# Optimization experiments

Measured on AMD Instinct MI355X. Metric: run time of the kernel, lower is better.

Reference implementation:

```python
import jax, jax.numpy as jnp
import numpy as np

N = 50000
E = 1600000
IN = 128
HID = 128
OUT = 64
NL = 200000
NEG_SLOPE = 0.2


def _glorot(key, shape):
    fan_in, fan_out = shape[0], shape[-1]
    s = jnp.sqrt(6.0 / (fan_in + fan_out))
    return jax.random.uniform(key, shape, jnp.float32, -s, s)


def setup_inputs() -> dict:
    key = jax.random.key(0)
    ks = jax.random.split(key, 16)
    x = jax.random.normal(ks[0], (N, IN), jnp.float32)
    edge_index = jax.random.randint(ks[1], (2, E), 0, N, dtype=jnp.int32)
    edge_label_index = jax.random.randint(ks[2], (2, NL), 0, N, dtype=jnp.int32)
    return {
        "x": x,
        "edge_index": edge_index,
        "edge_label_index": edge_label_index,
        "W1": _glorot(ks[3], (IN, HID)),  "a1s": _glorot(ks[4], (HID,)),  "a1d": _glorot(ks[5], (HID,)),  "b1": jnp.zeros((HID,), jnp.float32),
        "W2": _glorot(ks[6], (HID, HID)), "a2s": _glorot(ks[7], (HID,)),  "a2d": _glorot(ks[8], (HID,)),  "b2": jnp.zeros((HID,), jnp.float32),
        "W3": _glorot(ks[9], (HID, HID)), "a3s": _glorot(ks[10], (HID,)), "a3d": _glorot(ks[11], (HID,)), "b3": jnp.zeros((HID,), jnp.float32),
        "W4": _glorot(ks[12], (HID, OUT)), "b4": jnp.zeros((OUT,), jnp.float32),
    }


def _add_self_loops(edge_index, n):
    loop = jnp.arange(n, dtype=edge_index.dtype)
    return jnp.concatenate([edge_index, jnp.stack([loop, loop])], axis=1)


def gat_conv(x, edge_index, W, a_s, a_d, b):
    """PyG GATConv, heads=1, add_self_loops=True: gather, LeakyReLU score,
    segment softmax over destination nodes, scatter-add aggregate."""
    n = x.shape[0]
    ei = _add_self_loops(edge_index, n)
    src, dst = ei[0], ei[1]
    h = x @ W                                    # [N, H]
    e = jax.nn.leaky_relu((h @ a_s)[src] + (h @ a_d)[dst], NEG_SLOPE)  # [E']
    m = jax.ops.segment_max(e, dst, num_segments=n)
    p = jnp.exp(e - m[dst])
    s = jax.ops.segment_sum(p, dst, num_segments=n)
    alpha = p / s[dst]                           # segment softmax
    out = jax.ops.segment_sum(h[src] * alpha[:, None], dst, num_segments=n)
    return out + b


def gcn_conv(x, edge_index, W, b):
    """PyG GCNConv: self-loops + symmetric degree normalization."""
    n = x.shape[0]
    ei = _add_self_loops(edge_index, n)
    src, dst = ei[0], ei[1]
    h = x @ W
    deg = jax.ops.segment_sum(jnp.ones(src.shape, h.dtype), dst, num_segments=n)
    dinv = jax.lax.rsqrt(deg)
    norm = dinv[src] * dinv[dst]                 # [E']
    out = jax.ops.segment_sum(h[src] * norm[:, None], dst, num_segments=n)
    return out + b


def reference(x, edge_index, edge_label_index,
              W1, a1s, a1d, b1, W2, a2s, a2d, b2,
              W3, a3s, a3d, b3, W4, b4):
    h = jax.nn.relu(gat_conv(x, edge_index, W1, a1s, a1d, b1))
    h = jax.nn.relu(gat_conv(h, edge_index, W2, a2s, a2d, b2))
    h = jax.nn.relu(gat_conv(h, edge_index, W3, a3s, a3d, b3))
    z = gcn_conv(h, edge_index, W4, b4)          # [N, OUT]
    # decode: dot product of endpoint embeddings -> link logits [NL]
    return (z[edge_label_index[0]] * z[edge_label_index[1]]).sum(axis=-1)
```

## Files before the change

kernel.cpp:

```cpp
#include <hip/hip_runtime.h>
#include <hip/hip_fp16.h>
#include <math.h>

#define NN   50000
#define NE   1600000
#define DHID 128
#define DOUTC 64
#define NLBL 200000
#define CAP  80
#define NEG  0.2f
#define NBK  196
#define CAPB 8800
#define CHK  4096

typedef unsigned short u16;


__global__ __launch_bounds__(256) void k_zero(int* __restrict__ gcnt) {
    int i = threadIdx.x;
    if (i < NBK) gcnt[i] = 0;
}

__global__ __launch_bounds__(256) void k_bin(const int* __restrict__ ei,
                                             int* __restrict__ gcnt,
                                             unsigned* __restrict__ bins) {
    __shared__ int cntL[NBK];
    __shared__ int curL[NBK];
    const int tid = threadIdx.x;
    const int e0 = blockIdx.x * CHK + tid * 16;
    const bool act = (e0 + 15) < NE;

    unsigned pk[16];
    int bb[16];
    if (act) {
#pragma unroll
        for (int g = 0; g < 4; ++g) {
            int4 s4 = *(const int4*)&ei[e0 + g * 4];
            int4 d4 = *(const int4*)&ei[NE + e0 + g * 4];
            int sa[4] = {s4.x, s4.y, s4.z, s4.w};
            int da[4] = {d4.x, d4.y, d4.z, d4.w};
#pragma unroll
            for (int k = 0; k < 4; ++k) {
                int idx = g * 4 + k;
                bb[idx] = da[k] >> 8;
                pk[idx] = (unsigned)sa[k] | ((unsigned)(da[k] & 255) << 16);
            }
        }
    }
    for (int i = tid; i < NBK; i += 256) cntL[i] = 0;
    __syncthreads();
    if (act) {
#pragma unroll
        for (int k = 0; k < 16; ++k) atomicAdd(&cntL[bb[k]], 1);
    }
    __syncthreads();
    for (int i = tid; i < NBK; i += 256) curL[i] = atomicAdd(&gcnt[i], cntL[i]);
    __syncthreads();
    if (act) {
#pragma unroll
        for (int k = 0; k < 16; ++k) {
            int off = atomicAdd(&curL[bb[k]], 1);
            bins[(size_t)bb[k] * CAPB + off] = pk[k];
        }
    }
}

__global__ __launch_bounds__(256) void k_build(const unsigned* __restrict__ bins,
                                               const int* __restrict__ gcnt,
                                               int* __restrict__ cnt,
                                               u16* __restrict__ csr) {
    __shared__ u16 rows[256 * CAP];
    __shared__ int cur[256];
    const int b = blockIdx.x, tid = threadIdx.x;
    const int d0 = b << 8;
    const int nd = min(256, NN - d0);
    if (tid < nd) { cur[tid] = 1; rows[tid * CAP] = (u16)(d0 + tid); }
    __syncthreads();
    const int n = gcnt[b];
    for (int i = tid; i < n; i += 256) {
        unsigned v = bins[(size_t)b * CAPB + i];
        int s = v & 0xFFFF, dl = v >> 16;
        int pos = atomicAdd(&cur[dl], 1);
        if (pos < CAP) rows[dl * CAP + pos] = (u16)s;
    }
    __syncthreads();
    const unsigned* rw = (const unsigned*)rows;
    unsigned* cw = (unsigned*)(csr + (size_t)d0 * CAP);
    const int tot = nd * (CAP / 2);
    for (int i = tid; i < tot; i += 256) cw[i] = rw[i];
    if (tid < nd) cnt[d0 + tid] = cur[tid];
}


template <int NOUT, bool ATTN>
__global__ __launch_bounds__(256) void gemm_k(const float* __restrict__ A,
                                              const float* __restrict__ W,
                                              __half* __restrict__ C16,
                                              const float* __restrict__ a_s,
                                              const float* __restrict__ a_d,
                                              float* __restrict__ asv,
                                              float* __restrict__ adv, int M) {
    constexpr int BM = 64, BK = 32, TM = 4, TN = NOUT / 16;
    __shared__ float As[BM][36];
    __shared__ float Ws[BK][NOUT];
    const int tid = threadIdx.x;
    const int tx = tid & 15, ty = tid >> 4;
    const int row0 = blockIdx.x * BM;

    float acc[TM][TN];
#pragma unroll
    for (int i = 0; i < TM; ++i)
#pragma unroll
        for (int j = 0; j < TN; ++j) acc[i][j] = 0.f;

    for (int k0 = 0; k0 < 128; k0 += BK) {
        {
            int r = tid >> 3;
            int c = (tid & 7) * 4;
#pragma unroll
            for (int rr = 0; rr < BM; rr += 32) {
                int grow = row0 + r + rr;
                float4 v = make_float4(0.f, 0.f, 0.f, 0.f);
                if (grow < M) v = *(const float4*)&A[(size_t)grow * 128 + k0 + c];
                *(float4*)&As[r + rr][c] = v;
            }
        }
        {
            constexpr int TOT4 = BK * NOUT / 4;
#pragma unroll
            for (int i4 = tid; i4 < TOT4; i4 += 256) {
                int kk = (i4 * 4) / NOUT;
                int cc = (i4 * 4) % NOUT;
                *(float4*)&Ws[kk][cc] = *(const float4*)&W[(size_t)(k0 + kk) * NOUT + cc];
            }
        }
        __syncthreads();
#pragma unroll
        for (int k4 = 0; k4 < BK; k4 += 4) {
            float a4[TM][4];
#pragma unroll
            for (int i = 0; i < TM; ++i) {
                float4 v = *(const float4*)&As[ty * TM + i][k4];
                a4[i][0] = v.x; a4[i][1] = v.y; a4[i][2] = v.z; a4[i][3] = v.w;
            }
#pragma unroll
            for (int kk = 0; kk < 4; ++kk) {
                int k = k4 + kk;
                float rw[TN];
                if (NOUT == 128) {
                    float4 w0 = *(const float4*)&Ws[k][tx * 4];
                    float4 w1 = *(const float4*)&Ws[k][64 + tx * 4];
                    rw[0] = w0.x; rw[1] = w0.y; rw[2] = w0.z; rw[3] = w0.w;
                    rw[4] = w1.x; rw[5] = w1.y; rw[6] = w1.z; rw[7] = w1.w;
                } else {
                    float4 w0 = *(const float4*)&Ws[k][tx * 4];
                    rw[0] = w0.x; rw[1] = w0.y; rw[2] = w0.z; rw[3] = w0.w;
                }
#pragma unroll
                for (int i = 0; i < TM; ++i)
#pragma unroll
                    for (int j = 0; j < TN; ++j) acc[i][j] = fmaf(a4[i][kk], rw[j], acc[i][j]);
            }
        }
        __syncthreads();
    }
#pragma unroll
    for (int i = 0; i < TM; ++i) {
        int grow = row0 + ty * TM + i;
        if (grow < M) {
            __half2 p0 = __floats2half2_rn(acc[i][0], acc[i][1]);
            __half2 p1 = __floats2half2_rn(acc[i][2], acc[i][3]);
            __half2* cp = (__half2*)&C16[(size_t)grow * NOUT + tx * 4];
            cp[0] = p0; cp[1] = p1;
            if (NOUT == 128) {
                __half2 p2 = __floats2half2_rn(acc[i][4], acc[i][5]);
                __half2 p3 = __floats2half2_rn(acc[i][6], acc[i][7]);
                __half2* cq = (__half2*)&C16[(size_t)grow * NOUT + 64 + tx * 4];
                cq[0] = p2; cq[1] = p3;
            }
        }
    }
    if (ATTN) {
        float4 s0 = *(const float4*)&a_s[tx * 4];
        float4 s1 = *(const float4*)&a_s[64 + tx * 4];
        float4 d0 = *(const float4*)&a_d[tx * 4];
        float4 d1 = *(const float4*)&a_d[64 + tx * 4];
#pragma unroll
        for (int i = 0; i < TM; ++i) {
            float ps = acc[i][0] * s0.x + acc[i][1] * s0.y + acc[i][2] * s0.z + acc[i][3] * s0.w
                     + acc[i][4] * s1.x + acc[i][5] * s1.y + acc[i][6] * s1.z + acc[i][7] * s1.w;
            float pd = acc[i][0] * d0.x + acc[i][1] * d0.y + acc[i][2] * d0.z + acc[i][3] * d0.w
                     + acc[i][4] * d1.x + acc[i][5] * d1.y + acc[i][6] * d1.z + acc[i][7] * d1.w;
#pragma unroll
            for (int off = 1; off < 16; off <<= 1) {
                ps += __shfl_xor(ps, off);
                pd += __shfl_xor(pd, off);
            }
            int grow = row0 + ty * TM + i;
            if (tx == 0 && grow < M) { asv[grow] = ps; adv[grow] = pd; }
        }
    }
}

__device__ inline void fma_h8(uint4 u, float al, float* acc) {
    float2 f0 = __half22float2(*(__half2*)&u.x);
    float2 f1 = __half22float2(*(__half2*)&u.y);
    float2 f2 = __half22float2(*(__half2*)&u.z);
    float2 f3 = __half22float2(*(__half2*)&u.w);
    acc[0] = fmaf(al, f0.x, acc[0]);
    acc[1] = fmaf(al, f0.y, acc[1]);
    acc[2] = fmaf(al, f1.x, acc[2]);
    acc[3] = fmaf(al, f1.y, acc[3]);
    acc[4] = fmaf(al, f2.x, acc[4]);
    acc[5] = fmaf(al, f2.y, acc[5]);
    acc[6] = fmaf(al, f3.x, acc[6]);
    acc[7] = fmaf(al, f3.y, acc[7]);
}


__global__ __launch_bounds__(256) void k_gat_agg(const __half* __restrict__ h,
                                                 const int* __restrict__ cnt,
                                                 const u16* __restrict__ csr,
                                                 const float* __restrict__ asv,
                                                 const float* __restrict__ adv,
                                                 const float* __restrict__ bias,
                                                 float* __restrict__ outp) {
    int lane = threadIdx.x & 63, wv = threadIdx.x >> 6;
    int d = blockIdx.x * 4 + wv;
    if (d >= NN) return;
    int deg = cnt[d]; if (deg > CAP) deg = CAP;
    const float advd = adv[d];
    const u16* rowp = csr + (size_t)d * CAP;

    int j0 = lane, j1 = lane + 64;
    int s0 = 0, s1 = 0;
    float e0 = -INFINITY, e1 = -INFINITY;
    if (j0 < deg) {
        s0 = rowp[j0];
        float t = asv[s0] + advd;
        e0 = (t >= 0.f) ? t : NEG * t;
    }
    if (j1 < deg) {
        s1 = rowp[j1];
        float t = asv[s1] + advd;
        e1 = (t >= 0.f) ? t : NEG * t;
    }
    float m = fmaxf(e0, e1);
#pragma unroll
    for (int off = 32; off; off >>= 1) m = fmaxf(m, __shfl_xor(m, off));
    float p0 = (j0 < deg) ? __expf(e0 - m) : 0.f;
    float p1 = (j1 < deg) ? __expf(e1 - m) : 0.f;
    float s = p0 + p1;
#pragma unroll
    for (int off = 32; off; off >>= 1) s += __shfl_xor(s, off);
    float inv = 1.f / s;
    float a0 = p0 * inv, a1 = p1 * inv;

    int slot = lane >> 3, r = lane & 7;
    float acc[16];
#pragma unroll
    for (int k = 0; k < 16; ++k) acc[k] = 0.f;

    for (int base = 0; base < deg; base += 8) {
        int idx = base + slot;
        int lsrc = idx & 63;
        float alA = __shfl(a0, lsrc);
        float alB = __shfl(a1, lsrc);
        int   sjA = __shfl(s0, lsrc);
        int   sjB = __shfl(s1, lsrc);
        bool ok = idx < deg;
        float al = ok ? ((idx < 64) ? alA : alB) : 0.f;
        int   sj = ok ? ((idx < 64) ? sjA : sjB) : 0;
        const uint4* hp = (const uint4*)&h[(size_t)sj * 128 + r * 16];
        uint4 ua = hp[0];
        uint4 ub = hp[1];
        fma_h8(ua, al, acc);
        fma_h8(ub, al, acc + 8);
    }
#pragma unroll
    for (int k = 0; k < 16; ++k) {
        acc[k] += __shfl_xor(acc[k], 8);
        acc[k] += __shfl_xor(acc[k], 16);
        acc[k] += __shfl_xor(acc[k], 32);
    }
    if (slot == 0) {
        float o[16];
#pragma unroll
        for (int k = 0; k < 16; ++k) o[k] = fmaxf(acc[k] + bias[r * 16 + k], 0.f);
        float4* op = (float4*)&outp[(size_t)d * 128 + r * 16];
        op[0] = make_float4(o[0],  o[1],  o[2],  o[3]);
        op[1] = make_float4(o[4],  o[5],  o[6],  o[7]);
        op[2] = make_float4(o[8],  o[9],  o[10], o[11]);
        op[3] = make_float4(o[12], o[13], o[14], o[15]);
    }
}


__global__ __launch_bounds__(256) void k_gcn_agg(const __half* __restrict__ h,
                                                 const int* __restrict__ cnt,
                                                 const u16* __restrict__ csr,
                                                 const float* __restrict__ bias,
                                                 float* __restrict__ z) {
    int lane = threadIdx.x & 63, wv = threadIdx.x >> 6;
    int d = blockIdx.x * 4 + wv;
    if (d >= NN) return;
    int degc = cnt[d];
    int deg = degc > CAP ? CAP : degc;
    float did = rsqrtf((float)degc);
    const u16* rowp = csr + (size_t)d * CAP;

    int j0 = lane, j1 = lane + 64;
    int s0 = 0, s1 = 0;
    float n0 = 0.f, n1 = 0.f;
    if (j0 < deg) { s0 = rowp[j0]; n0 = rsqrtf((float)cnt[s0]) * did; }
    if (j1 < deg) { s1 = rowp[j1]; n1 = rsqrtf((float)cnt[s1]) * did; }

    int slot = lane >> 3, r = lane & 7;
    float acc[8];
#pragma unroll
    for (int k = 0; k < 8; ++k) acc[k] = 0.f;

    for (int base = 0; base < deg; base += 8) {
        int idx = base + slot;
        int lsrc = idx & 63;
        float nA = __shfl(n0, lsrc);
        float nB = __shfl(n1, lsrc);
        int  sjA = __shfl(s0, lsrc);
        int  sjB = __shfl(s1, lsrc);
        bool ok = idx < deg;
        float nm = ok ? ((idx < 64) ? nA : nB) : 0.f;
        int   sj = ok ? ((idx < 64) ? sjA : sjB) : 0;
        uint4 u = *(const uint4*)&h[(size_t)sj * 64 + r * 8];
        fma_h8(u, nm, acc);
    }
#pragma unroll
    for (int k = 0; k < 8; ++k) {
        acc[k] += __shfl_xor(acc[k], 8);
        acc[k] += __shfl_xor(acc[k], 16);
        acc[k] += __shfl_xor(acc[k], 32);
    }
    if (slot == 0) {
        float4 b0 = *(const float4*)&bias[r * 8];
        float4 b1 = *(const float4*)&bias[r * 8 + 4];
        float4* zp = (float4*)&z[(size_t)d * 64 + r * 8];
        zp[0] = make_float4(acc[0] + b0.x, acc[1] + b0.y, acc[2] + b0.z, acc[3] + b0.w);
        zp[1] = make_float4(acc[4] + b1.x, acc[5] + b1.y, acc[6] + b1.z, acc[7] + b1.w);
    }
}


__global__ __launch_bounds__(256) void k_decode(const float* __restrict__ z,
                                                const int* __restrict__ eli,
                                                float* __restrict__ outp) {
    int lane = threadIdx.x & 63, wv = threadIdx.x >> 6;
    int g = lane >> 4, r = lane & 15;
    int idx = (blockIdx.x * 4 + wv) * 4 + g;
    if (idx >= NLBL) return;
    int a = eli[idx], b = eli[NLBL + idx];
    float4 za = *(const float4*)&z[(size_t)a * 64 + r * 4];
    float4 zb = *(const float4*)&z[(size_t)b * 64 + r * 4];
    float v = za.x * zb.x + za.y * zb.y + za.z * zb.z + za.w * zb.w;
#pragma unroll
    for (int off = 8; off; off >>= 1) v += __shfl_xor(v, off);
    if (r == 0) outp[idx] = v;
}


extern "C" void kernel_launch(void* const* d_in, const int* in_sizes, int n_in,
                              void* d_out, int out_size, void* d_ws, size_t ws_size,
                              hipStream_t stream) {
    const float* x   = (const float*)d_in[0];
    const int*   ei  = (const int*)d_in[1];
    const int*   eli = (const int*)d_in[2];
    const float* W1 = (const float*)d_in[3];
    const float* a1s = (const float*)d_in[4];
    const float* a1d = (const float*)d_in[5];
    const float* b1 = (const float*)d_in[6];
    const float* W2 = (const float*)d_in[7];
    const float* a2s = (const float*)d_in[8];
    const float* a2d = (const float*)d_in[9];
    const float* b2 = (const float*)d_in[10];
    const float* W3 = (const float*)d_in[11];
    const float* a3s = (const float*)d_in[12];
    const float* a3d = (const float*)d_in[13];
    const float* b3 = (const float*)d_in[14];
    const float* W4 = (const float*)d_in[15];
    const float* b4 = (const float*)d_in[16];
    float* outp = (float*)d_out;

    char* p = (char*)d_ws;
    auto alloc = [&](size_t bytes) -> char* {
        char* r = p;
        p += (bytes + 255) & ~(size_t)255;
        return r;
    };
    int*   cnt  = (int*)alloc((size_t)NN * 4);
    u16*   csr  = (u16*)alloc((size_t)NN * CAP * 2);
    int*   gcnt = (int*)alloc((size_t)NBK * 4);
    float* asv  = (float*)alloc((size_t)NN * 4);
    float* advv = (float*)alloc((size_t)NN * 4);
    __half* G   = (__half*)alloc((size_t)NN * 128 * 2);
    float* Bu1  = (float*)alloc((size_t)NN * 128 * 4);
    float* Bu2  = (float*)alloc((size_t)NN * 128 * 4);
    unsigned* bins = (unsigned*)Bu2;

    const int gBin  = (NE + CHK - 1) / CHK;
    const int gGemm = (NN + 63) / 64;
    const int gNode = (NN + 3) / 4;
    const int gDec  = (NLBL + 15) / 16;

    k_zero<<<1, 256, 0, stream>>>(gcnt);
    k_bin<<<gBin, 256, 0, stream>>>(ei, gcnt, bins);
    k_build<<<NBK, 256, 0, stream>>>(bins, gcnt, cnt, csr);

    gemm_k<128, true><<<gGemm, 256, 0, stream>>>(x, W1, G, a1s, a1d, asv, advv, NN);
    k_gat_agg<<<gNode, 256, 0, stream>>>(G, cnt, csr, asv, advv, b1, Bu1);

    gemm_k<128, true><<<gGemm, 256, 0, stream>>>(Bu1, W2, G, a2s, a2d, asv, advv, NN);
    k_gat_agg<<<gNode, 256, 0, stream>>>(G, cnt, csr, asv, advv, b2, Bu2);

    gemm_k<128, true><<<gGemm, 256, 0, stream>>>(Bu2, W3, G, a3s, a3d, asv, advv, NN);
    k_gat_agg<<<gNode, 256, 0, stream>>>(G, cnt, csr, asv, advv, b3, Bu1);

    gemm_k<64, false><<<gGemm, 256, 0, stream>>>(Bu1, W4, G, nullptr, nullptr, nullptr, nullptr, NN);
    k_gcn_agg<<<gNode, 256, 0, stream>>>(G, cnt, csr, b4, Bu2);

    k_decode<<<gDec, 256, 0, stream>>>(Bu2, eli, outp);
}
```

Measured before the change: 455.6 us.

## Use fp16 MFMA for dense transforms and store layer activations in half

Replaces the scalar FP32 tiled GEMM with a kernel that puts the transposed weights in shared memory as fp16 and computes with 16x16x32 f16 MFMA instructions, keeping the fused attention-score reduction. The input features are cast to fp16 by a new kernel, and GAT aggregation outputs are written as fp16, which halves the activation traffic between layers. The aim is to remove FP32 ALU-bound GEMM time and reduce memory bandwidth. In exchange it adds a cast pass and lowers the precision of the inputs and intermediates.

New measurement: 444.1 us. 1.03x faster.

```diff
diff --git a/kernel.cpp b/kernel.cpp
--- a/kernel.cpp
+++ b/kernel.cpp
@@ -14,6 +14,8 @@
 #define CHK  4096
 
 typedef unsigned short u16;
+typedef _Float16 half8 __attribute__((ext_vector_type(8)));
+typedef float floatx4 __attribute__((ext_vector_type(4)));
 
 
 __global__ __launch_bounds__(256) void k_zero(int* __restrict__ gcnt) {
@@ -92,112 +94,104 @@
 }
 
 
+__global__ __launch_bounds__(256) void k_cast(const float* __restrict__ x,
+                                              __half* __restrict__ x16) {
+    int i = (blockIdx.x * 256 + threadIdx.x) * 4;
+    if (i < NN * 128) {
+        float4 v = *(const float4*)&x[i];
+        __half2 h0 = __floats2half2_rn(v.x, v.y);
+        __half2 h1 = __floats2half2_rn(v.z, v.w);
+        uint2 u;
+        __builtin_memcpy(&u.x, &h0, 4);
+        __builtin_memcpy(&u.y, &h1, 4);
+        *(uint2*)&x16[i] = u;
+    }
+}
+
+
 template <int NOUT, bool ATTN>
-__global__ __launch_bounds__(256) void gemm_k(const float* __restrict__ A,
-                                              const float* __restrict__ W,
-                                              __half* __restrict__ C16,
-                                              const float* __restrict__ a_s,
-                                              const float* __restrict__ a_d,
-                                              float* __restrict__ asv,
-                                              float* __restrict__ adv, int M) {
-    constexpr int BM = 64, BK = 32, TM = 4, TN = NOUT / 16;
-    __shared__ float As[BM][36];
-    __shared__ float Ws[BK][NOUT];
+__global__ __launch_bounds__(256) void gemm_mfma(const __half* __restrict__ A16,
+                                                 const float* __restrict__ W,
+                                                 __half* __restrict__ C16,
+                                                 const float* __restrict__ a_s,
+                                                 const float* __restrict__ a_d,
+                                                 float* __restrict__ asv,
+                                                 float* __restrict__ adv, int M) {
+    constexpr int CT = NOUT / 16;
+    __shared__ _Float16 Wt[NOUT][136];
     const int tid = threadIdx.x;
-    const int tx = tid & 15, ty = tid >> 4;
-    const int row0 = blockIdx.x * BM;
-
-    float acc[TM][TN];
-#pragma unroll
-    for (int i = 0; i < TM; ++i)
-#pragma unroll
-        for (int j = 0; j < TN; ++j) acc[i][j] = 0.f;
-
-    for (int k0 = 0; k0 < 128; k0 += BK) {
-        {
-            int r = tid >> 3;
-            int c = (tid & 7) * 4;
-#pragma unroll
-            for (int rr = 0; rr < BM; rr += 32) {
-                int grow = row0 + r + rr;
-                float4 v = make_float4(0.f, 0.f, 0.f, 0.f);
-                if (grow < M) v = *(const float4*)&A[(size_t)grow * 128 + k0 + c];
-                *(float4*)&As[r + rr][c] = v;
+    for (int i4 = tid; i4 < 128 * NOUT / 4; i4 += 256) {
+        int i = i4 * 4;
+        int k = i / NOUT, n = i % NOUT;
+        float4 w = *(const float4*)&W[i];
+        Wt[n + 0][k] = (_Float16)w.x;
+        Wt[n + 1][k] = (_Float16)w.y;
+        Wt[n + 2][k] = (_Float16)w.z;
+        Wt[n + 3][k] = (_Float16)w.w;
+    }
+    __syncthreads();
+
+    const int wave = tid >> 6, lane = tid & 63;
+    const int n = lane & 15, quad = lane >> 4;
+    const int row0 = blockIdx.x * 64 + wave * 16;
+
+    half8 a[4];
+    const bool rowok = (row0 + n) < M;
+    const _Float16* Ap = (const _Float16*)A16 + (size_t)(row0 + n) * 128 + quad * 8;
+    half8 zz = {};
+#pragma unroll
+    for (int ks = 0; ks < 4; ++ks)
+        a[ks] = rowok ? *(const half8*)(Ap + ks * 32) : zz;
+
+    floatx4 acc[CT];
+#pragma unroll
+    for (int c = 0; c < CT; ++c) acc[c] = (floatx4){0.f, 0.f, 0.f, 0.f};
+
+#pragma unroll
+    for (int c = 0; c < CT; ++c) {
+#pragma unroll
+        for (int ks = 0; ks < 4; ++ks) {
+            half8 b = *(const half8*)&Wt[c * 16 + n][ks * 32 + quad * 8];
+            acc[c] = __builtin_amdgcn_mfma_f32_16x16x32_f16(a[ks], b, acc[c], 0, 0, 0);
+        }
+    }
+
+#pragma unroll
+    for (int c = 0; c < CT; ++c) {
+#pragma unroll
+        for (int reg = 0; reg < 4; ++reg) {
+            int row = row0 + quad * 4 + reg;
+            if (row < M) C16[(size_t)row * NOUT + c * 16 + n] = __float2half(acc[c][reg]);
+        }
+    }
+
+    if (ATTN) {
+        float ps[4] = {0.f, 0.f, 0.f, 0.f};
+        float pd[4] = {0.f, 0.f, 0.f, 0.f};
+#pragma unroll
+        for (int c = 0; c < CT; ++c) {
+            float sv = a_s[c * 16 + n];
+            float dv = a_d[c * 16 + n];
+#pragma unroll
+            for (int reg = 0; reg < 4; ++reg) {
+                ps[reg] = fmaf(acc[c][reg], sv, ps[reg]);
+                pd[reg] = fmaf(acc[c][reg], dv, pd[reg]);
             }
         }
-        {
-            constexpr int TOT4 = BK * NOUT / 4;
-#pragma unroll
-            for (int i4 = tid; i4 < TOT4; i4 += 256) {
-                int kk = (i4 * 4) / NOUT;
-                int cc = (i4 * 4) % NOUT;
-                *(float4*)&Ws[kk][cc] = *(const float4*)&W[(size_t)(k0 + kk) * NOUT + cc];
+#pragma unroll
+        for (int off = 1; off < 16; off <<= 1) {
+#pragma unroll
+            for (int reg = 0; reg < 4; ++reg) {
+                ps[reg] += __shfl_xor(ps[reg], off);
+                pd[reg] += __shfl_xor(pd[reg], off);
             }
         }
-        __syncthreads();
-#pragma unroll
-        for (int k4 = 0; k4 < BK; k4 += 4) {
-            float a4[TM][4];
-#pragma unroll
-            for (int i = 0; i < TM; ++i) {
-                float4 v = *(const float4*)&As[ty * TM + i][k4];
-                a4[i][0] = v.x; a4[i][1] = v.y; a4[i][2] = v.z; a4[i][3] = v.w;
+        if (n == 0) {
+#pragma unroll
+            for (int reg = 0; reg < 4; ++reg) {
+                int row = row0 + quad * 4 + reg;
+                if (row < M) { asv[row] = ps[reg]; adv[row] = pd[reg]; }
             }
-#pragma unroll
-            for (int kk = 0; kk < 4; ++kk) {
-                int k = k4 + kk;
-                float rw[TN];
-                if (NOUT == 128) {
-                    float4 w0 = *(const float4*)&Ws[k][tx * 4];
-                    float4 w1 = *(const float4*)&Ws[k][64 + tx * 4];
-                    rw[0] = w0.x; rw[1] = w0.y; rw[2] = w0.z; rw[3] = w0.w;
-                    rw[4] = w1.x; rw[5] = w1.y; rw[6] = w1.z; rw[7] = w1.w;
-                } else {
-                    float4 w0 = *(const float4*)&Ws[k][tx * 4];
-                    rw[0] = w0.x; rw[1] = w0.y; rw[2] = w0.z; rw[3] = w0.w;
-                }
-#pragma unroll
-                for (int i = 0; i < TM; ++i)
-#pragma unroll
-                    for (int j = 0; j < TN; ++j) acc[i][j] = fmaf(a4[i][kk], rw[j], acc[i][j]);
-            }
-        }
-        __syncthreads();
-    }
-#pragma unroll
-    for (int i = 0; i < TM; ++i) {
-        int grow = row0 + ty * TM + i;
-        if (grow < M) {
-            __half2 p0 = __floats2half2_rn(acc[i][0], acc[i][1]);
-            __half2 p1 = __floats2half2_rn(acc[i][2], acc[i][3]);
-            __half2* cp = (__half2*)&C16[(size_t)grow * NOUT + tx * 4];
-            cp[0] = p0; cp[1] = p1;
-            if (NOUT == 128) {
-                __half2 p2 = __floats2half2_rn(acc[i][4], acc[i][5]);
-                __half2 p3 = __floats2half2_rn(acc[i][6], acc[i][7]);
-                __half2* cq = (__half2*)&C16[(size_t)grow * NOUT + 64 + tx * 4];
-                cq[0] = p2; cq[1] = p3;
-            }
-        }
-    }
-    if (ATTN) {
-        float4 s0 = *(const float4*)&a_s[tx * 4];
-        float4 s1 = *(const float4*)&a_s[64 + tx * 4];
-        float4 d0 = *(const float4*)&a_d[tx * 4];
-        float4 d1 = *(const float4*)&a_d[64 + tx * 4];
-#pragma unroll
-        for (int i = 0; i < TM; ++i) {
-            float ps = acc[i][0] * s0.x + acc[i][1] * s0.y + acc[i][2] * s0.z + acc[i][3] * s0.w
-                     + acc[i][4] * s1.x + acc[i][5] * s1.y + acc[i][6] * s1.z + acc[i][7] * s1.w;
-            float pd = acc[i][0] * d0.x + acc[i][1] * d0.y + acc[i][2] * d0.z + acc[i][3] * d0.w
-                     + acc[i][4] * d1.x + acc[i][5] * d1.y + acc[i][6] * d1.z + acc[i][7] * d1.w;
-#pragma unroll
-            for (int off = 1; off < 16; off <<= 1) {
-                ps += __shfl_xor(ps, off);
-                pd += __shfl_xor(pd, off);
-            }
-            int grow = row0 + ty * TM + i;
-            if (tx == 0 && grow < M) { asv[grow] = ps; adv[grow] = pd; }
         }
     }
 }
@@ -224,7 +218,7 @@
                                                  const float* __restrict__ asv,
                                                  const float* __restrict__ adv,
                                                  const float* __restrict__ bias,
-                                                 float* __restrict__ outp) {
+                                                 __half* __restrict__ outp) {
     int lane = threadIdx.x & 63, wv = threadIdx.x >> 6;
     int d = blockIdx.x * 4 + wv;
     if (d >= NN) return;
@@ -284,14 +278,18 @@
         acc[k] += __shfl_xor(acc[k], 32);
     }
     if (slot == 0) {
-        float o[16];
-#pragma unroll
-        for (int k = 0; k < 16; ++k) o[k] = fmaxf(acc[k] + bias[r * 16 + k], 0.f);
-        float4* op = (float4*)&outp[(size_t)d * 128 + r * 16];
-        op[0] = make_float4(o[0],  o[1],  o[2],  o[3]);
-        op[1] = make_float4(o[4],  o[5],  o[6],  o[7]);
-        op[2] = make_float4(o[8],  o[9],  o[10], o[11]);
-        op[3] = make_float4(o[12], o[13], o[14], o[15]);
+        __half2 ho[8];
+#pragma unroll
+        for (int k = 0; k < 8; ++k) {
+            float oa = fmaxf(acc[2 * k]     + bias[r * 16 + 2 * k],     0.f);
+            float ob = fmaxf(acc[2 * k + 1] + bias[r * 16 + 2 * k + 1], 0.f);
+            ho[k] = __floats2half2_rn(oa, ob);
+        }
+        uint4 u0, u1;
+        __builtin_memcpy(&u0, &ho[0], 16);
+        __builtin_memcpy(&u1, &ho[4], 16);
+        uint4* op = (uint4*)&outp[(size_t)d * 128 + r * 16];
+        op[0] = u0; op[1] = u1;
     }
 }
 
@@ -394,17 +392,20 @@
         p += (bytes + 255) & ~(size_t)255;
         return r;
     };
-    int*   cnt  = (int*)alloc((size_t)NN * 4);
-    u16*   csr  = (u16*)alloc((size_t)NN * CAP * 2);
-    int*   gcnt = (int*)alloc((size_t)NBK * 4);
-    float* asv  = (float*)alloc((size_t)NN * 4);
-    float* advv = (float*)alloc((size_t)NN * 4);
-    __half* G   = (__half*)alloc((size_t)NN * 128 * 2);
-    float* Bu1  = (float*)alloc((size_t)NN * 128 * 4);
-    float* Bu2  = (float*)alloc((size_t)NN * 128 * 4);
-    unsigned* bins = (unsigned*)Bu2;
+    int*    cnt  = (int*)alloc((size_t)NN * 4);
+    u16*    csr  = (u16*)alloc((size_t)NN * CAP * 2);
+    int*    gcnt = (int*)alloc((size_t)NBK * 4);
+    float*  asv  = (float*)alloc((size_t)NN * 4);
+    float*  advv = (float*)alloc((size_t)NN * 4);
+    __half* x16  = (__half*)alloc((size_t)NN * 128 * 2);
+    __half* G    = (__half*)alloc((size_t)NN * 128 * 2);
+    __half* Bu1  = (__half*)alloc((size_t)NN * 128 * 2);
+    __half* Bu2  = (__half*)alloc((size_t)NN * 128 * 2);
+    float*  zf   = (float*)alloc((size_t)NN * 64 * 4);
+    unsigned* bins = (unsigned*)alloc((size_t)NBK * CAPB * 4);
 
     const int gBin  = (NE + CHK - 1) / CHK;
+    const int gCast = (NN * 128 / 4 + 255) / 256;
     const int gGemm = (NN + 63) / 64;
     const int gNode = (NN + 3) / 4;
     const int gDec  = (NLBL + 15) / 16;
@@ -412,18 +413,19 @@
     k_zero<<<1, 256, 0, stream>>>(gcnt);
     k_bin<<<gBin, 256, 0, stream>>>(ei, gcnt, bins);
     k_build<<<NBK, 256, 0, stream>>>(bins, gcnt, cnt, csr);
-
-    gemm_k<128, true><<<gGemm, 256, 0, stream>>>(x, W1, G, a1s, a1d, asv, advv, NN);
+    k_cast<<<gCast, 256, 0, stream>>>(x, x16);
+
+    gemm_mfma<128, true><<<gGemm, 256, 0, stream>>>(x16, W1, G, a1s, a1d, asv, advv, NN);
     k_gat_agg<<<gNode, 256, 0, stream>>>(G, cnt, csr, asv, advv, b1, Bu1);
 
-    gemm_k<128, true><<<gGemm, 256, 0, stream>>>(Bu1, W2, G, a2s, a2d, asv, advv, NN);
+    gemm_mfma<128, true><<<gGemm, 256, 0, stream>>>(Bu1, W2, G, a2s, a2d, asv, advv, NN);
     k_gat_agg<<<gNode, 256, 0, stream>>>(G, cnt, csr, asv, advv, b2, Bu2);
 
-    gemm_k<128, true><<<gGemm, 256, 0, stream>>>(Bu2, W3, G, a3s, a3d, asv, advv, NN);
+    gemm_mfma<128, true><<<gGemm, 256, 0, stream>>>(Bu2, W3, G, a3s, a3d, asv, advv, NN);
     k_gat_agg<<<gNode, 256, 0, stream>>>(G, cnt, csr, asv, advv, b3, Bu1);
 
-    gemm_k<64, false><<<gGemm, 256, 0, stream>>>(Bu1, W4, G, nullptr, nullptr, nullptr, nullptr, NN);
-    k_gcn_agg<<<gNode, 256, 0, stream>>>(G, cnt, csr, b4, Bu2);
-
-    k_decode<<<gDec, 256, 0, stream>>>(Bu2, eli, outp);
-}
+    gemm_mfma<64, false><<<gGemm, 256, 0, stream>>>(Bu1, W4, G, nullptr, nullptr, nullptr, nullptr, NN);
+    k_gcn_agg<<<gNode, 256, 0, stream>>>(G, cnt, csr, b4, zf);
+
+    k_decode<<<gDec, 256, 0, stream>>>(zf, eli, outp);
+}
```
